# Kernel tuning notes

Hardware: AMD Instinct MI355X
Metric: run time of the kernel (lower is better)

Reference implementation:

```python
import jax, jax.numpy as jnp
import numpy as np

IN_FEATURES = 2048
OUT_FEATURES = 2048
BATCH = 4096


def setup_inputs() -> dict:
    key = jax.random.key(0)
    kx, kw, kb, kp = jax.random.split(key, 4)
    x = jax.random.normal(kx, (BATCH, IN_FEATURES), dtype=jnp.float32)
    weight = jax.random.normal(kw, (OUT_FEATURES, IN_FEATURES), dtype=jnp.float32)
    bias = jax.random.normal(kb, (OUT_FEATURES,), dtype=jnp.float32)
    # torch uses torch.randperm(in_features) at forward time; we fix a permutation here
    indices = jax.random.permutation(kp, IN_FEATURES).astype(jnp.int64)
    return {"x": x, "weight": weight, "bias": bias, "indices": indices}


def reference(x, weight, bias, indices):
    # Original: (x[:, None, :] * weight)[:, :, indices].sum(dim=2) + bias
    # Summing the permuted reduction axis == contracting the permuted operands;
    # we gather both x and weight along the permutation then do a real GEMM,
    # avoiding the huge [B, out, in] intermediate while keeping identical math.
    xp = x[:, indices]            # [B, in]
    wp = weight[:, indices]       # [out, in]
    return jnp.einsum('bi,oi->bo', xp, wp) + bias[None, :]
```

## Files before the change

### kernel.cpp

```cpp
#include <hip/hip_runtime.h>
#include <hip/hip_bf16.h>

#define M_DIM 4096
#define N_DIM 2048
#define K_DIM 2048

#define BM 256
#define BN 128
#define BK 64
#define NT (K_DIM / BK)
#define A_TILE (BM * BK)
#define B_TILE (BN * BK)

typedef __bf16 bf16x8 __attribute__((ext_vector_type(8)));
typedef float f32x4 __attribute__((ext_vector_type(4)));
typedef unsigned short u16x8 __attribute__((ext_vector_type(8)));

__device__ __forceinline__ unsigned short f32_to_bf16_rne(float f) {
  unsigned int u = __float_as_uint(f);
  u += 0x7fffu + ((u >> 16) & 1u);
  return (unsigned short)(u >> 16);
}

__global__ __launch_bounds__(256) void cvt_both(
    const float* __restrict__ x, const float* __restrict__ w,
    unsigned short* __restrict__ out, int xn8, int totn8) {
  int i = blockIdx.x * 256 + threadIdx.x;
  if (i >= totn8) return;
  const float* src = (i < xn8) ? (x + (size_t)i * 8)
                               : (w + (size_t)(i - xn8) * 8);
  f32x4 a = reinterpret_cast<const f32x4*>(src)[0];
  f32x4 b = reinterpret_cast<const f32x4*>(src)[1];
  u16x8 o;
  o[0] = f32_to_bf16_rne(a[0]); o[1] = f32_to_bf16_rne(a[1]);
  o[2] = f32_to_bf16_rne(a[2]); o[3] = f32_to_bf16_rne(a[3]);
  o[4] = f32_to_bf16_rne(b[0]); o[5] = f32_to_bf16_rne(b[1]);
  o[6] = f32_to_bf16_rne(b[2]); o[7] = f32_to_bf16_rne(b[3]);
  reinterpret_cast<u16x8*>(out)[i] = o;
}

__device__ __forceinline__ void gload_lds16(const unsigned short* g, unsigned short* l) {
  __builtin_amdgcn_global_load_lds(
      (const __attribute__((address_space(1))) unsigned int*)g,
      (__attribute__((address_space(3))) unsigned int*)l, 16, 0, 0);
}

#define LD8(p) (*reinterpret_cast<const bf16x8*>(p))
#define VMWAIT_(n) asm volatile("s_waitcnt vmcnt(" #n ")" ::: "memory")
#define VMWAIT(n) VMWAIT_(n)
#define SBAR() __builtin_amdgcn_s_barrier()
#define SCHED() __builtin_amdgcn_sched_barrier(0)

__global__ __launch_bounds__(512, 2) void gemm_8w(
    const unsigned short* __restrict__ A,
    const unsigned short* __restrict__ B,
    const float* __restrict__ bias,
    float* __restrict__ C) {
  __shared__ unsigned short As[3 * A_TILE];
  __shared__ unsigned short Bs[3 * B_TILE];

  const int tid  = threadIdx.x;
  const int lane = tid & 63;
  const int wave = tid >> 6;
  const int wr   = wave >> 1;
  const int wc   = wave & 1;
  const int bn   = blockIdx.x;
  const int bm   = blockIdx.y;

  const int srow   = tid >> 3;
  const int schunk = (tid & 7) ^ (srow & 7);
  const unsigned short* Ag[4];
  const unsigned short* Bg[2];
#pragma unroll
  for (int j = 0; j < 4; ++j)
    Ag[j] = A + (size_t)(bm * BM + j * 64 + srow) * K_DIM + schunk * 8;
#pragma unroll
  for (int j = 0; j < 2; ++j)
    Bg[j] = B + (size_t)(bn * BN + j * 64 + srow) * K_DIM + schunk * 8;

#define STAGE_ALL(buf, k0) do { \
    unsigned short* _da = &As[(buf) * A_TILE + tid * 8]; \
    unsigned short* _db = &Bs[(buf) * B_TILE + tid * 8]; \
    gload_lds16(Ag[0] + (k0), _da); \
    gload_lds16(Ag[1] + (k0), _da + 4096); \
    gload_lds16(Ag[2] + (k0), _da + 8192); \
    gload_lds16(Ag[3] + (k0), _da + 12288); \
    gload_lds16(Bg[0] + (k0), _db); \
    gload_lds16(Bg[1] + (k0), _db + 4096); \
  } while (0)

  const int fr = lane & 15;
  const int qq = lane >> 4;
  const int xr = fr & 7;
  int aoff[4][2], boff[4][2];
#pragma unroll
  for (int mi = 0; mi < 4; ++mi)
#pragma unroll
    for (int kk = 0; kk < 2; ++kk)
      aoff[mi][kk] = ((wr * 64 + mi * 16 + fr) * 8 + ((kk * 4 + qq) ^ xr)) * 8;
#pragma unroll
  for (int ni = 0; ni < 4; ++ni)
#pragma unroll
    for (int kk = 0; kk < 2; ++kk)
      boff[ni][kk] = ((wc * 64 + ni * 16 + fr) * 8 + ((kk * 4 + qq) ^ xr)) * 8;

  const f32x4 z = {0.f, 0.f, 0.f, 0.f};
  f32x4 acc[4][4];
#pragma unroll
  for (int i = 0; i < 4; ++i)
#pragma unroll
    for (int j = 0; j < 4; ++j) acc[i][j] = z;

  bf16x8 avA[4], bvA[4], avB[4], bvB[4];

#define READ_SET(av, bv, bufi, kk) do { \
    const unsigned short* Asb = &As[(bufi) * A_TILE]; \
    const unsigned short* Bsb = &Bs[(bufi) * B_TILE]; \
    bv[0] = LD8(Bsb + boff[0][kk]); bv[1] = LD8(Bsb + boff[1][kk]); \
    bv[2] = LD8(Bsb + boff[2][kk]); bv[3] = LD8(Bsb + boff[3][kk]); \
    av[0] = LD8(Asb + aoff[0][kk]); av[1] = LD8(Asb + aoff[1][kk]); \
    av[2] = LD8(Asb + aoff[2][kk]); av[3] = LD8(Asb + aoff[3][kk]); \
  } while (0)

#define MFMA_ALL(av, bv) do { \
    __builtin_amdgcn_s_setprio(1); \
    _Pragma("unroll") \
    for (int mi = 0; mi < 4; ++mi) { \
      acc[mi][0] = __builtin_amdgcn_mfma_f32_16x16x32_bf16(av[mi], bv[0], acc[mi][0], 0, 0, 0); \
      acc[mi][1] = __builtin_amdgcn_mfma_f32_16x16x32_bf16(av[mi], bv[1], acc[mi][1], 0, 0, 0); \
      acc[mi][2] = __builtin_amdgcn_mfma_f32_16x16x32_bf16(av[mi], bv[2], acc[mi][2], 0, 0, 0); \
      acc[mi][3] = __builtin_amdgcn_mfma_f32_16x16x32_bf16(av[mi], bv[3], acc[mi][3], 0, 0, 0); \
    } \
    __builtin_amdgcn_s_setprio(0); \
  } while (0)

#define TILE_MAIN(bufi, stgbufi, stgt) do { \
    STAGE_ALL(stgbufi, (stgt) * BK); \
    READ_SET(avB, bvB, bufi, 1); \
    SCHED(); \
    MFMA_ALL(avA, bvA); \
    SCHED(); \
    VMWAIT(6); \
    SBAR(); \
    SCHED(); \
    READ_SET(avA, bvA, ((bufi) + 1) % 3, 0); \
    SCHED(); \
    MFMA_ALL(avB, bvB); \
    SBAR(); \
    SCHED(); \
  } while (0)

  STAGE_ALL(0, 0);
  STAGE_ALL(1, BK);
  VMWAIT(6);
  SBAR();
  SCHED();
  READ_SET(avA, bvA, 0, 0);
  SCHED();

#pragma unroll 1
  for (int s = 0; s < 10; ++s) {
    const int t0 = s * 3;
    TILE_MAIN(0, 2, t0 + 2);
    TILE_MAIN(1, 0, t0 + 3);
    TILE_MAIN(2, 1, t0 + 4);
  }

  READ_SET(avB, bvB, 0, 1);
  SCHED();
  MFMA_ALL(avA, bvA);
  SCHED();
  VMWAIT(0);
  SBAR();
  SCHED();
  READ_SET(avA, bvA, 1, 0);
  SCHED();
  MFMA_ALL(avB, bvB);
  READ_SET(avB, bvB, 1, 1);
  SCHED();
  MFMA_ALL(avA, bvA);
  MFMA_ALL(avB, bvB);

  const int orow0 = bm * BM + wr * 64 + qq * 4;
  const int ocol0 = bn * BN + wc * 64 + fr;
#pragma unroll
  for (int ni = 0; ni < 4; ++ni) {
    const int col = ocol0 + ni * 16;
    const float bv = bias[col];
#pragma unroll
    for (int mi = 0; mi < 4; ++mi) {
      const int row = orow0 + mi * 16;
#pragma unroll
      for (int r = 0; r < 4; ++r)
        C[(size_t)(row + r) * N_DIM + col] = acc[mi][ni][r] + bv;
    }
  }
#undef TILE_MAIN
#undef MFMA_ALL
#undef READ_SET
#undef STAGE_ALL
}

__global__ __launch_bounds__(256) void gemm_f32_naive(
    const float* __restrict__ X, const float* __restrict__ W,
    const float* __restrict__ bias, float* __restrict__ C) {
  int o = blockIdx.x * 256 + threadIdx.x;
  if (o >= M_DIM * N_DIM) return;
  int m = o / N_DIM, n = o % N_DIM;
  const float* xr = X + (size_t)m * K_DIM;
  const float* wr = W + (size_t)n * K_DIM;
  float s = 0.f;
  for (int k = 0; k < K_DIM; ++k) s += xr[k] * wr[k];
  C[o] = s + bias[n];
}

extern "C" void kernel_launch(void* const* d_in, const int* in_sizes, int n_in,
                              void* d_out, int out_size, void* d_ws, size_t ws_size,
                              hipStream_t stream) {
  const float* x    = (const float*)d_in[0];
  const float* w    = (const float*)d_in[1];
  const float* bias = (const float*)d_in[2];
  float* out = (float*)d_out;

  const size_t x_elems = (size_t)M_DIM * K_DIM;
  const size_t w_elems = (size_t)N_DIM * K_DIM;
  const size_t need = (x_elems + w_elems) * sizeof(unsigned short);

  if (ws_size < need) {
    gemm_f32_naive<<<(M_DIM * N_DIM + 255) / 256, 256, 0, stream>>>(x, w, bias, out);
    return;
  }

  unsigned short* xb = (unsigned short*)d_ws;
  unsigned short* wb = xb + x_elems;

  const int xn8 = (int)(x_elems / 8);
  const int totn8 = (int)((x_elems + w_elems) / 8);
  cvt_both<<<(totn8 + 255) / 256, 256, 0, stream>>>(x, w, xb, xn8, totn8);

  dim3 grid(N_DIM / BN, M_DIM / BM);
  gemm_8w<<<grid, 512, 0, stream>>>(xb, wb, bias, out);
}
```

Before: 55.52 us.

## Switch GEMM to 128x128 tiles with 4 waves and double-buffered LDS

Shrinks the block tile from 256x128 with 8 waves to 128x128 with 4 waves and replaces the triple-buffered LDS pipeline with a simpler double buffer that waits for all loads each k-step. The smaller tile doubles the grid and cuts LDS per block, which may raise occupancy and balance work across CUs. The cost is lower operand reuse per tile, more global traffic, and a full vmcnt(0) wait plus one barrier per tile, which exposes load latency.

```diff
diff --git a/kernel.cpp b/kernel.cpp
--- a/kernel.cpp
+++ b/kernel.cpp
@@ -5,7 +5,7 @@
 #define N_DIM 2048
 #define K_DIM 2048
 
-#define BM 256
+#define BM 128
 #define BN 128
 #define BK 64
 #define NT (K_DIM / BK)
@@ -51,13 +51,13 @@
 #define SBAR() __builtin_amdgcn_s_barrier()
 #define SCHED() __builtin_amdgcn_sched_barrier(0)
 
-__global__ __launch_bounds__(512, 2) void gemm_8w(
+__global__ __launch_bounds__(256, 2) void gemm_db(
     const unsigned short* __restrict__ A,
     const unsigned short* __restrict__ B,
     const float* __restrict__ bias,
     float* __restrict__ C) {
-  __shared__ unsigned short As[3 * A_TILE];
-  __shared__ unsigned short Bs[3 * B_TILE];
+  __shared__ unsigned short As[2 * A_TILE];
+  __shared__ unsigned short Bs[2 * B_TILE];
 
   const int tid  = threadIdx.x;
   const int lane = tid & 63;
@@ -70,23 +70,24 @@
   const int srow   = tid >> 3;
   const int schunk = (tid & 7) ^ (srow & 7);
   const unsigned short* Ag[4];
-  const unsigned short* Bg[2];
-#pragma unroll
-  for (int j = 0; j < 4; ++j)
-    Ag[j] = A + (size_t)(bm * BM + j * 64 + srow) * K_DIM + schunk * 8;
-#pragma unroll
-  for (int j = 0; j < 2; ++j)
-    Bg[j] = B + (size_t)(bn * BN + j * 64 + srow) * K_DIM + schunk * 8;
+  const unsigned short* Bg[4];
+#pragma unroll
+  for (int j = 0; j < 4; ++j) {
+    Ag[j] = A + (size_t)(bm * BM + j * 32 + srow) * K_DIM + schunk * 8;
+    Bg[j] = B + (size_t)(bn * BN + j * 32 + srow) * K_DIM + schunk * 8;
+  }
 
 #define STAGE_ALL(buf, k0) do { \
     unsigned short* _da = &As[(buf) * A_TILE + tid * 8]; \
     unsigned short* _db = &Bs[(buf) * B_TILE + tid * 8]; \
     gload_lds16(Ag[0] + (k0), _da); \
-    gload_lds16(Ag[1] + (k0), _da + 4096); \
-    gload_lds16(Ag[2] + (k0), _da + 8192); \
-    gload_lds16(Ag[3] + (k0), _da + 12288); \
+    gload_lds16(Ag[1] + (k0), _da + 2048); \
+    gload_lds16(Ag[2] + (k0), _da + 4096); \
+    gload_lds16(Ag[3] + (k0), _da + 6144); \
     gload_lds16(Bg[0] + (k0), _db); \
-    gload_lds16(Bg[1] + (k0), _db + 4096); \
+    gload_lds16(Bg[1] + (k0), _db + 2048); \
+    gload_lds16(Bg[2] + (k0), _db + 4096); \
+    gload_lds16(Bg[3] + (k0), _db + 6144); \
   } while (0)
 
   const int fr = lane & 15;
@@ -134,48 +135,32 @@
     __builtin_amdgcn_s_setprio(0); \
   } while (0)
 
-#define TILE_MAIN(bufi, stgbufi, stgt) do { \
-    STAGE_ALL(stgbufi, (stgt) * BK); \
-    READ_SET(avB, bvB, bufi, 1); \
+#define TILE(p_, t_) do { \
+    STAGE_ALL((p_) ^ 1, ((t_) + 1) * BK); \
+    READ_SET(avB, bvB, p_, 1); \
     SCHED(); \
     MFMA_ALL(avA, bvA); \
+    MFMA_ALL(avB, bvB); \
     SCHED(); \
-    VMWAIT(6); \
+    VMWAIT(0); \
     SBAR(); \
     SCHED(); \
-    READ_SET(avA, bvA, ((bufi) + 1) % 3, 0); \
-    SCHED(); \
-    MFMA_ALL(avB, bvB); \
-    SBAR(); \
-    SCHED(); \
+    READ_SET(avA, bvA, (p_) ^ 1, 0); \
   } while (0)
 
   STAGE_ALL(0, 0);
-  STAGE_ALL(1, BK);
-  VMWAIT(6);
+  VMWAIT(0);
   SBAR();
   SCHED();
   READ_SET(avA, bvA, 0, 0);
-  SCHED();
 
 #pragma unroll 1
-  for (int s = 0; s < 10; ++s) {
-    const int t0 = s * 3;
-    TILE_MAIN(0, 2, t0 + 2);
-    TILE_MAIN(1, 0, t0 + 3);
-    TILE_MAIN(2, 1, t0 + 4);
-  }
-
-  READ_SET(avB, bvB, 0, 1);
-  SCHED();
-  MFMA_ALL(avA, bvA);
-  SCHED();
-  VMWAIT(0);
-  SBAR();
-  SCHED();
-  READ_SET(avA, bvA, 1, 0);
-  SCHED();
-  MFMA_ALL(avB, bvB);
+  for (int s = 0; s < 15; ++s) {
+    TILE(0, 2 * s);
+    TILE(1, 2 * s + 1);
+  }
+  TILE(0, 30);
+
   READ_SET(avB, bvB, 1, 1);
   SCHED();
   MFMA_ALL(avA, bvA);
@@ -195,7 +180,7 @@
         C[(size_t)(row + r) * N_DIM + col] = acc[mi][ni][r] + bv;
     }
   }
-#undef TILE_MAIN
+#undef TILE
 #undef MFMA_ALL
 #undef READ_SET
 #undef STAGE_ALL
@@ -239,5 +224,5 @@
   cvt_both<<<(totn8 + 255) / 256, 256, 0, stream>>>(x, w, xb, xn8, totn8);
 
   dim3 grid(N_DIM / BN, M_DIM / BM);
-  gemm_8w<<<grid, 512, 0, stream>>>(xb, wb, bias, out);
-}
+  gemm_db<<<grid, 256, 0, stream>>>(xb, wb, bias, out);
+}
```

Result: faster. 53.34 us (-3.9%).
